# Optimization experiments

Measured on AMD Instinct MI355X. Metric: run time of the kernel, lower is better.

## Reference

```python
import jax, jax.numpy as jnp
import numpy as np

H = 2048
EPS = 1e-5

def _layernorm(x, g, b):
    mu = jnp.mean(x, axis=-1, keepdims=True)
    var = jnp.mean(jnp.square(x - mu), axis=-1, keepdims=True)
    return (x - mu) * jax.lax.rsqrt(var + EPS) * g + b

def setup_inputs() -> dict:
    key = jax.random.key(0)
    ks = jax.random.split(key, 12)
    s = 1.0 / np.sqrt(H)
    inp = {
        "x": jax.random.normal(ks[0], (2, 2048, H), dtype=jnp.float32),
        "ln1_g": jnp.ones((H,), jnp.float32),
        "ln1_b": jnp.zeros((H,), jnp.float32),
        "ln2_g": jnp.ones((H,), jnp.float32),
        "ln2_b": jnp.zeros((H,), jnp.float32),
        "qkv_w": jax.random.uniform(ks[1], (H, 3 * H), jnp.float32, -s, s),
        "qkv_b": jax.random.uniform(ks[2], (3 * H,), jnp.float32, -s, s),
        "out_w": jax.random.uniform(ks[3], (H, H), jnp.float32, -s, s),
        "out_b": jax.random.uniform(ks[4], (H,), jnp.float32, -s, s),
        "mlp_w1": jax.random.uniform(ks[5], (H, 4 * H), jnp.float32, -s, s),
        "mlp_b1": jax.random.uniform(ks[6], (4 * H,), jnp.float32, -s, s),
        "mlp_w2": jax.random.uniform(ks[7], (4 * H, H), jnp.float32, -1.0 / np.sqrt(4 * H), 1.0 / np.sqrt(4 * H)),
        "mlp_b2": jax.random.uniform(ks[8], (H,), jnp.float32, -1.0 / np.sqrt(4 * H), 1.0 / np.sqrt(4 * H)),
    }
    return inp

def reference(x, ln1_g, ln1_b, ln2_g, ln2_b, qkv_w, qkv_b, out_w, out_b, mlp_w1, mlp_b1, mlp_w2, mlp_b2):
    residual = x
    h = _layernorm(x, ln1_g, ln1_b)
    qkv = h @ qkv_w + qkv_b                      # [B,S,3H]
    q, k, v = jnp.split(qkv, 3, axis=-1)         # each [B,S,H] (single-head attention)
    scores = jnp.einsum('bsh,bth->bst', q, k) / jnp.sqrt(jnp.float32(H))
    attn = jax.nn.softmax(scores, axis=-1)
    attn_out = jnp.einsum('bst,bth->bsh', attn, v)
    attn_out = attn_out @ out_w + out_b
    x = residual + attn_out                      # dropout is identity in eval
    residual = x
    h = _layernorm(x, ln2_g, ln2_b)
    h = jax.nn.gelu(h @ mlp_w1 + mlp_b1, approximate=False)
    h = h @ mlp_w2 + mlp_b2
    return residual + h
```

## Files before the change

### kernel.cpp

```cpp
#include <hip/hip_runtime.h>
#include <hip/hip_bf16.h>
#include <math.h>

typedef __bf16 bf16_t;
typedef __bf16 bf16x8 __attribute__((ext_vector_type(8)));
typedef __bf16 bf16x4 __attribute__((ext_vector_type(4)));
typedef float  f32x4  __attribute__((ext_vector_type(4)));

enum { EPI_BF16_BIAS = 0, EPI_F32_SCALE = 1, EPI_BF16 = 2, EPI_F32_BIAS_RES = 3, EPI_BF16_BIAS_GELU = 4 };

__device__ __forceinline__ float gelu_exact(float v) {
  return 0.5f * v * (1.0f + erff(v * 0.7071067811865476f));
}

__device__ __forceinline__ void gld_lds16(const bf16_t* g, bf16_t* l) {
  __builtin_amdgcn_global_load_lds(
      (const __attribute__((address_space(1))) uint32_t*)(uintptr_t)g,
      (__attribute__((address_space(3))) uint32_t*)(uintptr_t)l, 16, 0, 0);
}

#define SB()    __builtin_amdgcn_s_barrier()
#define SCHED() __builtin_amdgcn_sched_barrier(0)
#define VMW0()  asm volatile("s_waitcnt vmcnt(0)" ::: "memory")

#define RD(base, rowbase, ks) \
  (*(const bf16x8*)((base) + ((rowbase) + lr) * 64 + (((((ks) << 2) | lg)) ^ (lr & 7)) * 8))

template<int EPI>
__global__ __launch_bounds__(512, 2) void tb_gemm8(
    const bf16_t* __restrict__ A, int lda, long long strideA,
    const bf16_t* __restrict__ B, int ldb, long long strideB,
    const float* __restrict__ bias,
    const float* __restrict__ resid,
    void* __restrict__ Cp, int ldc, long long strideC,
    int K, float scale)
{
  __shared__ __align__(16) bf16_t sm[65536];

  const int tid = threadIdx.x;
  const int lane = tid & 63;
  const int wid = tid >> 6;
  const int wm = wid >> 2;
  const int wn = wid & 3;
  const int lr = lane & 15;
  const int lg = lane >> 4;
  const int z = blockIdx.z;
  const int m0 = blockIdx.y * 256;
  const int n0 = blockIdx.x * 256;

  const bf16_t* Ag = A + (size_t)z * strideA + (size_t)m0 * lda;
  const bf16_t* Bg = B + (size_t)z * strideB + (size_t)n0 * ldb;

  const int l3 = lane >> 3;
  const int sl8 = ((lane & 7) ^ l3) << 3;

  f32x4 acc[8][4];
#pragma unroll
  for (int i = 0; i < 8; ++i)
#pragma unroll
    for (int j = 0; j < 4; ++j) acc[i][j] = (f32x4){0.f, 0.f, 0.f, 0.f};

  auto stage = [&](int par, int kt) {
    bf16_t* da = sm + (par << 15);
    bf16_t* db = da + 16384;
#pragma unroll
    for (int h = 0; h < 2; ++h)
#pragma unroll
      for (int q = 0; q < 2; ++q) {
        int c = (wid << 1) + q;
        int row = (h << 7) + (c << 3) + l3;
        gld_lds16(Ag + (size_t)row * lda + kt + sl8, da + (h << 13) + (c << 9) + lane * 8);
        gld_lds16(Bg + (size_t)row * ldb + kt + sl8, db + (h << 13) + (c << 9) + lane * 8);
      }
  };

  const int NT = K >> 6;
  stage(0, 0);
  VMW0();
  SB();

  for (int t = 0; t < NT; ++t) {
    SCHED();
    const bf16_t* cura = sm + ((t & 1) << 15);
    const bf16_t* curb = cura + 16384;
    if (t + 1 < NT) stage((t + 1) & 1, (t + 1) << 6);

    bf16x8 bF[4][2], aF[4][2];
#pragma unroll
    for (int jj = 0; jj < 4; ++jj) {
      bF[jj][0] = RD(curb, jj * 64 + wn * 16, 0);
      bF[jj][1] = RD(curb, jj * 64 + wn * 16, 1);
    }
#pragma unroll
    for (int ii = 0; ii < 4; ++ii) {
      aF[ii][0] = RD(cura, ii * 32 + wm * 16, 0);
      aF[ii][1] = RD(cura, ii * 32 + wm * 16, 1);
    }
    __builtin_amdgcn_s_setprio(1);
#pragma unroll
    for (int ii = 0; ii < 4; ++ii)
#pragma unroll
      for (int jj = 0; jj < 4; ++jj)
#pragma unroll
        for (int ks = 0; ks < 2; ++ks)
          acc[ii][jj] = __builtin_amdgcn_mfma_f32_16x16x32_bf16(aF[ii][ks], bF[jj][ks], acc[ii][jj], 0, 0, 0);
    __builtin_amdgcn_s_setprio(0);
#pragma unroll
    for (int ii = 0; ii < 4; ++ii) {
      aF[ii][0] = RD(cura, 128 + ii * 32 + wm * 16, 0);
      aF[ii][1] = RD(cura, 128 + ii * 32 + wm * 16, 1);
    }
    __builtin_amdgcn_s_setprio(1);
#pragma unroll
    for (int ii = 0; ii < 4; ++ii)
#pragma unroll
      for (int jj = 0; jj < 4; ++jj)
#pragma unroll
        for (int ks = 0; ks < 2; ++ks)
          acc[4 + ii][jj] = __builtin_amdgcn_mfma_f32_16x16x32_bf16(aF[ii][ks], bF[jj][ks], acc[4 + ii][jj], 0, 0, 0);
    __builtin_amdgcn_s_setprio(0);

    SCHED();
    if (t + 1 < NT) {
      VMW0();
      SB();
    }
  }

#pragma unroll
  for (int i = 0; i < 8; ++i) {
    const int mr = ((i >> 2) << 7) + ((i & 3) << 5) + (wm << 4);
#pragma unroll
    for (int j = 0; j < 4; ++j) {
      const int nc = j * 64 + (wn << 4);
#pragma unroll
      for (int r = 0; r < 4; ++r) {
        int row = m0 + mr + lg * 4 + r;
        int col = n0 + nc + lr;
        float v = acc[i][j][r] * scale;
        if constexpr (EPI == EPI_BF16_BIAS || EPI == EPI_F32_BIAS_RES || EPI == EPI_BF16_BIAS_GELU)
          v += bias[col];
        if constexpr (EPI == EPI_BF16_BIAS_GELU)
          v = gelu_exact(v);
        if constexpr (EPI == EPI_F32_BIAS_RES)
          v += resid[(size_t)row * ldc + col];
        if constexpr (EPI == EPI_BF16_BIAS || EPI == EPI_BF16 || EPI == EPI_BF16_BIAS_GELU) {
          ((bf16_t*)Cp)[(size_t)z * strideC + (size_t)row * ldc + col] = (bf16_t)v;
        } else {
          ((float*)Cp)[(size_t)z * strideC + (size_t)row * ldc + col] = v;
        }
      }
    }
  }
}

__global__ __launch_bounds__(256) void tb_combine(
    const float* __restrict__ x2, const float* __restrict__ p0,
    const float* __restrict__ p1, const float* __restrict__ bias,
    float* __restrict__ out)
{
  size_t o = ((size_t)blockIdx.x * 256 + threadIdx.x) * 4;
  float4 a = *(const float4*)(x2 + o);
  float4 b = *(const float4*)(p0 + o);
  float4 c = *(const float4*)(p1 + o);
  float4 bb = *(const float4*)(bias + (o & 2047));
  float4 r;
  r.x = a.x + b.x + c.x + bb.x;
  r.y = a.y + b.y + c.y + bb.y;
  r.z = a.z + b.z + c.z + bb.z;
  r.w = a.w + b.w + c.w + bb.w;
  *(float4*)(out + o) = r;
}

__global__ __launch_bounds__(256) void tb_transpose_cast(
    const float* __restrict__ in, bf16_t* __restrict__ outT, int R, int C)
{
  __shared__ float tile[32][33];
  int c0 = blockIdx.x * 32;
  int r0 = blockIdx.y * 32;
  int t = threadIdx.x;
  int r = t >> 3;
  int c4 = (t & 7) * 4;
  float4 d = *(const float4*)(in + (size_t)(r0 + r) * C + c0 + c4);
  tile[r][c4 + 0] = d.x; tile[r][c4 + 1] = d.y; tile[r][c4 + 2] = d.z; tile[r][c4 + 3] = d.w;
  __syncthreads();
  int c = t >> 3;
  int r4 = (t & 7) * 4;
  bf16x4 o;
  o[0] = (bf16_t)tile[r4 + 0][c];
  o[1] = (bf16_t)tile[r4 + 1][c];
  o[2] = (bf16_t)tile[r4 + 2][c];
  o[3] = (bf16_t)tile[r4 + 3][c];
  *(bf16x4*)(outT + (size_t)(c0 + c) * R + r0 + r4) = o;
}

__global__ __launch_bounds__(256) void tb_transpose_bf16(
    const bf16_t* __restrict__ in, int ldin, long long sIn,
    bf16_t* __restrict__ out, int ldout, long long sOut)
{
  __shared__ bf16_t tile[32][40];
  int z = blockIdx.z;
  const bf16_t* src = in + (size_t)z * sIn;
  bf16_t* dst = out + (size_t)z * sOut;
  int c0 = blockIdx.x * 32;
  int r0 = blockIdx.y * 32;
  int t = threadIdx.x;
  int r = t >> 3;
  int c4 = (t & 7) * 4;
  bf16x4 d = *(const bf16x4*)(src + (size_t)(r0 + r) * ldin + c0 + c4);
  *(bf16x4*)&tile[r][c4] = d;
  __syncthreads();
  int c = t >> 3;
  int r4 = (t & 7) * 4;
  bf16x4 o;
  o[0] = tile[r4 + 0][c];
  o[1] = tile[r4 + 1][c];
  o[2] = tile[r4 + 2][c];
  o[3] = tile[r4 + 3][c];
  *(bf16x4*)(dst + (size_t)(c0 + c) * ldout + r0 + r4) = o;
}

__global__ __launch_bounds__(256) void tb_layernorm(
    const float* __restrict__ x, const float* __restrict__ g, const float* __restrict__ b,
    bf16_t* __restrict__ h)
{
  __shared__ float sa[4], sb[4];
  int row = blockIdx.x;
  int t = threadIdx.x;
  const float* xr = x + (size_t)row * 2048;
  float4 v0 = *(const float4*)(xr + t * 8);
  float4 v1 = *(const float4*)(xr + t * 8 + 4);
  float a[8] = {v0.x, v0.y, v0.z, v0.w, v1.x, v1.y, v1.z, v1.w};
  float s = 0.f, q = 0.f;
#pragma unroll
  for (int j = 0; j < 8; ++j) { s += a[j]; q += a[j] * a[j]; }
#pragma unroll
  for (int o = 32; o; o >>= 1) { s += __shfl_down(s, o); q += __shfl_down(q, o); }
  int w = t >> 6, l = t & 63;
  if (l == 0) { sa[w] = s; sb[w] = q; }
  __syncthreads();
  if (t == 0) {
    sa[0] = sa[0] + sa[1] + sa[2] + sa[3];
    sb[0] = sb[0] + sb[1] + sb[2] + sb[3];
  }
  __syncthreads();
  float mu = sa[0] * (1.0f / 2048.0f);
  float var = sb[0] * (1.0f / 2048.0f) - mu * mu;
  float rs = rsqrtf(var + 1e-5f);
  float4 g0 = *(const float4*)(g + t * 8);
  float4 g1 = *(const float4*)(g + t * 8 + 4);
  float4 b0 = *(const float4*)(b + t * 8);
  float4 b1 = *(const float4*)(b + t * 8 + 4);
  float gv[8] = {g0.x, g0.y, g0.z, g0.w, g1.x, g1.y, g1.z, g1.w};
  float bv[8] = {b0.x, b0.y, b0.z, b0.w, b1.x, b1.y, b1.z, b1.w};
  bf16x8 o8;
#pragma unroll
  for (int j = 0; j < 8; ++j) o8[j] = (bf16_t)((a[j] - mu) * rs * gv[j] + bv[j]);
  *(bf16x8*)(h + (size_t)row * 2048 + t * 8) = o8;
}

__global__ __launch_bounds__(256) void tb_softmax(
    const float* __restrict__ S, bf16_t* __restrict__ P)
{
  __shared__ float sa[4];
  int row = blockIdx.x;
  int t = threadIdx.x;
  const float* sr = S + (size_t)row * 2048;
  float4 a0 = *(const float4*)(sr + t * 8);
  float4 a1 = *(const float4*)(sr + t * 8 + 4);
  float v[8] = {a0.x, a0.y, a0.z, a0.w, a1.x, a1.y, a1.z, a1.w};
  float m = v[0];
#pragma unroll
  for (int j = 1; j < 8; ++j) m = fmaxf(m, v[j]);
#pragma unroll
  for (int o = 32; o; o >>= 1) m = fmaxf(m, __shfl_down(m, o));
  int w = t >> 6, l = t & 63;
  if (l == 0) sa[w] = m;
  __syncthreads();
  if (t == 0) sa[0] = fmaxf(fmaxf(sa[0], sa[1]), fmaxf(sa[2], sa[3]));
  __syncthreads();
  m = sa[0];
  __syncthreads();
  float s = 0.f;
#pragma unroll
  for (int j = 0; j < 8; ++j) { v[j] = expf(v[j] - m); s += v[j]; }
#pragma unroll
  for (int o = 32; o; o >>= 1) s += __shfl_down(s, o);
  if (l == 0) sa[w] = s;
  __syncthreads();
  if (t == 0) sa[0] = sa[0] + sa[1] + sa[2] + sa[3];
  __syncthreads();
  float inv = 1.0f / sa[0];
  bf16x8 o8;
#pragma unroll
  for (int j = 0; j < 8; ++j) o8[j] = (bf16_t)(v[j] * inv);
  *(bf16x8*)(P + (size_t)row * 2048 + t * 8) = o8;
}

extern "C" void kernel_launch(void* const* d_in, const int* in_sizes, int n_in,
                              void* d_out, int out_size, void* d_ws, size_t ws_size,
                              hipStream_t stream) {
  const float* x     = (const float*)d_in[0];
  const float* ln1_g = (const float*)d_in[1];
  const float* ln1_b = (const float*)d_in[2];
  const float* ln2_g = (const float*)d_in[3];
  const float* ln2_b = (const float*)d_in[4];
  const float* qkv_w = (const float*)d_in[5];
  const float* qkv_b = (const float*)d_in[6];
  const float* out_w = (const float*)d_in[7];
  const float* out_b = (const float*)d_in[8];
  const float* w1    = (const float*)d_in[9];
  const float* b1    = (const float*)d_in[10];
  const float* w2    = (const float*)d_in[11];
  const float* b2    = (const float*)d_in[12];
  float* out = (float*)d_out;
  char* ws = (char*)d_ws;

  bf16_t* qkv_wT = (bf16_t*)(ws + 0);
  bf16_t* out_wT = (bf16_t*)(ws + 25165824);
  bf16_t* w1T    = (bf16_t*)(ws + 33554432);
  bf16_t* w2T    = (bf16_t*)(ws + 67108864);
  bf16_t* h_bf   = (bf16_t*)(ws + 100663296);
  bf16_t* qkv_bf = (bf16_t*)(ws + 117440512);
  float*  scores = (float*)(ws + 167772160);
  bf16_t* attn_bf= (bf16_t*)(ws + 201326592);
  bf16_t* ao_bf  = (bf16_t*)(ws + 218103808);
  float*  x2     = (float*)(ws + 234881024);
  bf16_t* mid_bf = (bf16_t*)(ws + 117440512);
  bf16_t* Vt     = (bf16_t*)(ws + 234881024);
  float*  part0  = (float*)(ws + 0);
  float*  part1  = (float*)(ws + 201326592);

  const float inv_sqrt_h = 0.022097086912079608f;

  tb_transpose_cast<<<dim3(6144 / 32, 2048 / 32), 256, 0, stream>>>(qkv_w, qkv_wT, 2048, 6144);
  tb_transpose_cast<<<dim3(2048 / 32, 2048 / 32), 256, 0, stream>>>(out_w, out_wT, 2048, 2048);
  tb_transpose_cast<<<dim3(8192 / 32, 2048 / 32), 256, 0, stream>>>(w1, w1T, 2048, 8192);
  tb_transpose_cast<<<dim3(2048 / 32, 8192 / 32), 256, 0, stream>>>(w2, w2T, 8192, 2048);

  tb_layernorm<<<4096, 256, 0, stream>>>(x, ln1_g, ln1_b, h_bf);

  tb_gemm8<EPI_BF16_BIAS><<<dim3(24, 16, 1), 512, 0, stream>>>(
      h_bf, 2048, 0, qkv_wT, 2048, 0, qkv_b, nullptr, qkv_bf, 6144, 0, 2048, 1.0f);

  tb_transpose_bf16<<<dim3(64, 64, 2), 256, 0, stream>>>(
      qkv_bf + 4096, 6144, 2048LL * 6144, Vt, 2048, 2048LL * 2048);

  tb_gemm8<EPI_F32_SCALE><<<dim3(8, 8, 2), 512, 0, stream>>>(
      qkv_bf, 6144, 2048LL * 6144, qkv_bf + 2048, 6144, 2048LL * 6144,
      nullptr, nullptr, scores, 2048, 2048LL * 2048, 2048, inv_sqrt_h);

  tb_softmax<<<4096, 256, 0, stream>>>(scores, attn_bf);

  tb_gemm8<EPI_BF16><<<dim3(8, 8, 2), 512, 0, stream>>>(
      attn_bf, 2048, 2048LL * 2048, Vt, 2048, 2048LL * 2048,
      nullptr, nullptr, ao_bf, 2048, 2048LL * 2048, 2048, 1.0f);

  tb_gemm8<EPI_F32_BIAS_RES><<<dim3(8, 16, 1), 512, 0, stream>>>(
      ao_bf, 2048, 0, out_wT, 2048, 0, out_b, x, x2, 2048, 0, 2048, 1.0f);

  tb_layernorm<<<4096, 256, 0, stream>>>(x2, ln2_g, ln2_b, h_bf);

  tb_gemm8<EPI_BF16_BIAS_GELU><<<dim3(32, 16, 1), 512, 0, stream>>>(
      h_bf, 2048, 0, w1T, 2048, 0, b1, nullptr, mid_bf, 8192, 0, 2048, 1.0f);

  tb_gemm8<EPI_F32_SCALE><<<dim3(8, 16, 2), 512, 0, stream>>>(
      mid_bf, 8192, 4096, w2T, 8192, 4096,
      nullptr, nullptr, part0, 2048, 50331648LL, 4096, 1.0f);

  tb_combine<<<8192, 256, 0, stream>>>(x2, part0, part1, b2, out);
}
```

Measured before the change: 734.5 us.

## Switch GEMM to a 4-stage LDS ring with K-tile 32 and unswizzled layout

Replaces the double-buffered 64-wide K pipeline with a four-slot ring of 32-wide K tiles, keeping three global-to-LDS loads in flight. Partial vmcnt waits (8/4/0) replace the full drain each step. The goal is to hide global-load latency better. In exchange it drops the XOR swizzle, so LDS reads may hit bank conflicts. It also issues twice as many barriers per unit of K.

```diff
diff --git a/kernel.cpp b/kernel.cpp
--- a/kernel.cpp
+++ b/kernel.cpp
@@ -21,10 +21,9 @@
 
 #define SB()    __builtin_amdgcn_s_barrier()
 #define SCHED() __builtin_amdgcn_sched_barrier(0)
+#define VMW8()  asm volatile("s_waitcnt vmcnt(8)" ::: "memory")
+#define VMW4()  asm volatile("s_waitcnt vmcnt(4)" ::: "memory")
 #define VMW0()  asm volatile("s_waitcnt vmcnt(0)" ::: "memory")
-
-#define RD(base, rowbase, ks) \
-  (*(const bf16x8*)((base) + ((rowbase) + lr) * 64 + (((((ks) << 2) | lg)) ^ (lr & 7)) * 8))
 
 template<int EPI>
 __global__ __launch_bounds__(512, 2) void tb_gemm8(
@@ -51,8 +50,8 @@
   const bf16_t* Ag = A + (size_t)z * strideA + (size_t)m0 * lda;
   const bf16_t* Bg = B + (size_t)z * strideB + (size_t)n0 * ldb;
 
-  const int l3 = lane >> 3;
-  const int sl8 = ((lane & 7) ^ l3) << 3;
+  const int srow = lane >> 2;
+  const int scol = (lane & 3) * 8;
 
   f32x4 acc[8][4];
 #pragma unroll
@@ -60,70 +59,52 @@
 #pragma unroll
     for (int j = 0; j < 4; ++j) acc[i][j] = (f32x4){0.f, 0.f, 0.f, 0.f};
 
-  auto stage = [&](int par, int kt) {
-    bf16_t* da = sm + (par << 15);
-    bf16_t* db = da + 16384;
-#pragma unroll
-    for (int h = 0; h < 2; ++h)
-#pragma unroll
-      for (int q = 0; q < 2; ++q) {
-        int c = (wid << 1) + q;
-        int row = (h << 7) + (c << 3) + l3;
-        gld_lds16(Ag + (size_t)row * lda + kt + sl8, da + (h << 13) + (c << 9) + lane * 8);
-        gld_lds16(Bg + (size_t)row * ldb + kt + sl8, db + (h << 13) + (c << 9) + lane * 8);
-      }
+  auto stage = [&](bf16_t* buf, int kt) {
+#pragma unroll
+    for (int q = 0; q < 2; ++q) {
+      int c = (wid << 1) + q;
+      int row = (c << 4) + srow;
+      gld_lds16(Ag + (size_t)row * lda + kt + scol, buf + (c << 9) + lane * 8);
+      gld_lds16(Bg + (size_t)row * ldb + kt + scol, buf + 8192 + (c << 9) + lane * 8);
+    }
   };
 
-  const int NT = K >> 6;
-  stage(0, 0);
-  VMW0();
+  const int NT = K >> 5;
+  stage(sm, 0);
+  stage(sm + 16384, 32);
+  stage(sm + 32768, 64);
+  VMW8();
   SB();
 
-  for (int t = 0; t < NT; ++t) {
-    SCHED();
-    const bf16_t* cura = sm + ((t & 1) << 15);
-    const bf16_t* curb = cura + 16384;
-    if (t + 1 < NT) stage((t + 1) & 1, (t + 1) << 6);
-
-    bf16x8 bF[4][2], aF[4][2];
-#pragma unroll
-    for (int jj = 0; jj < 4; ++jj) {
-      bF[jj][0] = RD(curb, jj * 64 + wn * 16, 0);
-      bF[jj][1] = RD(curb, jj * 64 + wn * 16, 1);
-    }
-#pragma unroll
-    for (int ii = 0; ii < 4; ++ii) {
-      aF[ii][0] = RD(cura, ii * 32 + wm * 16, 0);
-      aF[ii][1] = RD(cura, ii * 32 + wm * 16, 1);
-    }
-    __builtin_amdgcn_s_setprio(1);
-#pragma unroll
-    for (int ii = 0; ii < 4; ++ii)
+  for (int tb = 0; tb < NT; tb += 4) {
+#pragma unroll
+    for (int u = 0; u < 4; ++u) {
+      const int t = tb + u;
+      const bf16_t* ab = sm + u * 16384;
+      const bf16_t* bb = ab + 8192;
+      if (t + 3 < NT) stage(sm + ((u + 3) & 3) * 16384, (t + 3) << 5);
+
+      bf16x8 aF[8], bF[4];
 #pragma unroll
       for (int jj = 0; jj < 4; ++jj)
-#pragma unroll
-        for (int ks = 0; ks < 2; ++ks)
-          acc[ii][jj] = __builtin_amdgcn_mfma_f32_16x16x32_bf16(aF[ii][ks], bF[jj][ks], acc[ii][jj], 0, 0, 0);
-    __builtin_amdgcn_s_setprio(0);
-#pragma unroll
-    for (int ii = 0; ii < 4; ++ii) {
-      aF[ii][0] = RD(cura, 128 + ii * 32 + wm * 16, 0);
-      aF[ii][1] = RD(cura, 128 + ii * 32 + wm * 16, 1);
-    }
-    __builtin_amdgcn_s_setprio(1);
-#pragma unroll
-    for (int ii = 0; ii < 4; ++ii)
-#pragma unroll
-      for (int jj = 0; jj < 4; ++jj)
-#pragma unroll
-        for (int ks = 0; ks < 2; ++ks)
-          acc[4 + ii][jj] = __builtin_amdgcn_mfma_f32_16x16x32_bf16(aF[ii][ks], bF[jj][ks], acc[4 + ii][jj], 0, 0, 0);
-    __builtin_amdgcn_s_setprio(0);
-
-    SCHED();
-    if (t + 1 < NT) {
-      VMW0();
-      SB();
+        bF[jj] = *(const bf16x8*)&bb[(jj * 64 + wn * 16 + lr) * 32 + lg * 8];
+#pragma unroll
+      for (int ii = 0; ii < 8; ++ii)
+        aF[ii] = *(const bf16x8*)&ab[((((ii >> 2) << 7) + ((ii & 3) << 5) + (wm << 4)) + lr) * 32 + lg * 8];
+
+      __builtin_amdgcn_s_setprio(1);
+#pragma unroll
+      for (int ii = 0; ii < 8; ++ii)
+#pragma unroll
+        for (int jj = 0; jj < 4; ++jj)
+          acc[ii][jj] = __builtin_amdgcn_mfma_f32_16x16x32_bf16(aF[ii], bF[jj], acc[ii][jj], 0, 0, 0);
+      __builtin_amdgcn_s_setprio(0);
+
+      SCHED();
+      if (t + 3 < NT)      { VMW8(); SB(); }
+      else if (t == NT - 3) { VMW4(); SB(); }
+      else if (t == NT - 2) { VMW0(); SB(); }
+      SCHED();
     }
   }
 
```

After: 868.9 us. 1.18x slower.

## Split-K the attention and output-projection GEMMs to fill more CUs

Applied to the files above, without the earlier changes.

Adds a ZDIV template parameter to the GEMM so the z grid dimension covers batch times K-split, with per-split K offsets. QK^T, PV and the output projection now run as 2-way split-K with fp32 partial outputs. The partials are summed in softmax (now tb_softmax_add), in a new tb_combine_pv kernel, and in tb_combine for the residual. The aim is more workgroups on the small 64/128-tile grids for better CU occupancy, at the cost of extra fp32 partial traffic, an extra combine launch, and a rearranged workspace.

```diff
diff --git a/kernel.cpp b/kernel.cpp
--- a/kernel.cpp
+++ b/kernel.cpp
@@ -23,13 +23,10 @@
 #define SCHED() __builtin_amdgcn_sched_barrier(0)
 #define VMW0()  asm volatile("s_waitcnt vmcnt(0)" ::: "memory")
 
-#define RD(base, rowbase, ks) \
-  (*(const bf16x8*)((base) + ((rowbase) + lr) * 64 + (((((ks) << 2) | lg)) ^ (lr & 7)) * 8))
-
-template<int EPI>
+template<int EPI, int ZDIV>
 __global__ __launch_bounds__(512, 2) void tb_gemm8(
-    const bf16_t* __restrict__ A, int lda, long long strideA,
-    const bf16_t* __restrict__ B, int ldb, long long strideB,
+    const bf16_t* __restrict__ A, int lda, long long strideA, long long kofA,
+    const bf16_t* __restrict__ B, int ldb, long long strideB, long long kofB,
     const float* __restrict__ bias,
     const float* __restrict__ resid,
     void* __restrict__ Cp, int ldc, long long strideC,
@@ -45,11 +42,13 @@
   const int lr = lane & 15;
   const int lg = lane >> 4;
   const int z = blockIdx.z;
+  const int batch = z / ZDIV;
+  const int ks = z % ZDIV;
   const int m0 = blockIdx.y * 256;
   const int n0 = blockIdx.x * 256;
 
-  const bf16_t* Ag = A + (size_t)z * strideA + (size_t)m0 * lda;
-  const bf16_t* Bg = B + (size_t)z * strideB + (size_t)n0 * ldb;
+  const bf16_t* Ag = A + (size_t)batch * strideA + (size_t)ks * kofA + (size_t)m0 * lda;
+  const bf16_t* Bg = B + (size_t)batch * strideB + (size_t)ks * kofB + (size_t)n0 * ldb;
 
   const int l3 = lane >> 3;
   const int sl8 = ((lane & 7) ^ l3) << 3;
@@ -74,6 +73,9 @@
       }
   };
 
+#define RD(base, rowbase, kslot) \
+  (*(const bf16x8*)((base) + ((rowbase) + lr) * 64 + (((((kslot) << 2) | lg)) ^ (lr & 7)) * 8))
+
   const int NT = K >> 6;
   stage(0, 0);
   VMW0();
@@ -102,8 +104,8 @@
 #pragma unroll
       for (int jj = 0; jj < 4; ++jj)
 #pragma unroll
-        for (int ks = 0; ks < 2; ++ks)
-          acc[ii][jj] = __builtin_amdgcn_mfma_f32_16x16x32_bf16(aF[ii][ks], bF[jj][ks], acc[ii][jj], 0, 0, 0);
+        for (int kk = 0; kk < 2; ++kk)
+          acc[ii][jj] = __builtin_amdgcn_mfma_f32_16x16x32_bf16(aF[ii][kk], bF[jj][kk], acc[ii][jj], 0, 0, 0);
     __builtin_amdgcn_s_setprio(0);
 #pragma unroll
     for (int ii = 0; ii < 4; ++ii) {
@@ -116,8 +118,8 @@
 #pragma unroll
       for (int jj = 0; jj < 4; ++jj)
 #pragma unroll
-        for (int ks = 0; ks < 2; ++ks)
-          acc[4 + ii][jj] = __builtin_amdgcn_mfma_f32_16x16x32_bf16(aF[ii][ks], bF[jj][ks], acc[4 + ii][jj], 0, 0, 0);
+        for (int kk = 0; kk < 2; ++kk)
+          acc[4 + ii][jj] = __builtin_amdgcn_mfma_f32_16x16x32_bf16(aF[ii][kk], bF[jj][kk], acc[4 + ii][jj], 0, 0, 0);
     __builtin_amdgcn_s_setprio(0);
 
     SCHED();
@@ -126,6 +128,7 @@
       SB();
     }
   }
+#undef RD
 
 #pragma unroll
   for (int i = 0; i < 8; ++i) {
@@ -172,6 +175,24 @@
   *(float4*)(out + o) = r;
 }
 
+__global__ __launch_bounds__(256) void tb_combine_pv(
+    const float* __restrict__ p, bf16_t* __restrict__ ao)
+{
+  size_t o = ((size_t)blockIdx.x * 256 + threadIdx.x) * 4;
+  size_t b = o >> 22;
+  size_t w = o & 4194303;
+  const float* p0 = p + (b << 1) * 4194304 + w;
+  const float* p1 = p0 + 4194304;
+  float4 a = *(const float4*)p0;
+  float4 c = *(const float4*)p1;
+  bf16x4 r;
+  r[0] = (bf16_t)(a.x + c.x);
+  r[1] = (bf16_t)(a.y + c.y);
+  r[2] = (bf16_t)(a.z + c.z);
+  r[3] = (bf16_t)(a.w + c.w);
+  *(bf16x4*)(ao + o) = r;
+}
+
 __global__ __launch_bounds__(256) void tb_transpose_cast(
     const float* __restrict__ in, bf16_t* __restrict__ outT, int R, int C)
 {
@@ -259,16 +280,21 @@
   *(bf16x8*)(h + (size_t)row * 2048 + t * 8) = o8;
 }
 
-__global__ __launch_bounds__(256) void tb_softmax(
-    const float* __restrict__ S, bf16_t* __restrict__ P)
+__global__ __launch_bounds__(256) void tb_softmax_add(
+    const float* __restrict__ p, bf16_t* __restrict__ P)
 {
   __shared__ float sa[4];
   int row = blockIdx.x;
   int t = threadIdx.x;
-  const float* sr = S + (size_t)row * 2048;
-  float4 a0 = *(const float4*)(sr + t * 8);
-  float4 a1 = *(const float4*)(sr + t * 8 + 4);
-  float v[8] = {a0.x, a0.y, a0.z, a0.w, a1.x, a1.y, a1.z, a1.w};
+  size_t base = ((size_t)(row >> 11) * 2) * 4194304 + (size_t)(row & 2047) * 2048;
+  const float* p0 = p + base;
+  const float* p1 = p0 + 4194304;
+  float4 a0 = *(const float4*)(p0 + t * 8);
+  float4 a1 = *(const float4*)(p0 + t * 8 + 4);
+  float4 c0 = *(const float4*)(p1 + t * 8);
+  float4 c1 = *(const float4*)(p1 + t * 8 + 4);
+  float v[8] = {a0.x + c0.x, a0.y + c0.y, a0.z + c0.z, a0.w + c0.w,
+                a1.x + c1.x, a1.y + c1.y, a1.z + c1.z, a1.w + c1.w};
   float m = v[0];
 #pragma unroll
   for (int j = 1; j < 8; ++j) m = fmaxf(m, v[j]);
@@ -316,20 +342,18 @@
   float* out = (float*)d_out;
   char* ws = (char*)d_ws;
 
+  float*  sp     = (float*)(ws + 0);
   bf16_t* qkv_wT = (bf16_t*)(ws + 0);
-  bf16_t* out_wT = (bf16_t*)(ws + 25165824);
-  bf16_t* w1T    = (bf16_t*)(ws + 33554432);
-  bf16_t* w2T    = (bf16_t*)(ws + 67108864);
-  bf16_t* h_bf   = (bf16_t*)(ws + 100663296);
-  bf16_t* qkv_bf = (bf16_t*)(ws + 117440512);
-  float*  scores = (float*)(ws + 167772160);
-  bf16_t* attn_bf= (bf16_t*)(ws + 201326592);
-  bf16_t* ao_bf  = (bf16_t*)(ws + 218103808);
-  float*  x2     = (float*)(ws + 234881024);
-  bf16_t* mid_bf = (bf16_t*)(ws + 117440512);
-  bf16_t* Vt     = (bf16_t*)(ws + 234881024);
-  float*  part0  = (float*)(ws + 0);
-  float*  part1  = (float*)(ws + 201326592);
+  bf16_t* out_wT = (bf16_t*)(ws + 67108864);
+  bf16_t* w1T    = (bf16_t*)(ws + 75497472);
+  bf16_t* w2T    = (bf16_t*)(ws + 109051904);
+  bf16_t* h_bf   = (bf16_t*)(ws + 142606336);
+  bf16_t* qkv_bf = (bf16_t*)(ws + 159383552);
+  bf16_t* mid_bf = (bf16_t*)(ws + 159383552);
+  bf16_t* attn_bf= (bf16_t*)(ws + 209715200);
+  bf16_t* Vt     = (bf16_t*)(ws + 226492416);
+  bf16_t* ao_bf  = (bf16_t*)(ws + 243269632);
+  float*  x2     = (float*)(ws + 226492416);
 
   const float inv_sqrt_h = 0.022097086912079608f;
 
@@ -340,33 +364,38 @@
 
   tb_layernorm<<<4096, 256, 0, stream>>>(x, ln1_g, ln1_b, h_bf);
 
-  tb_gemm8<EPI_BF16_BIAS><<<dim3(24, 16, 1), 512, 0, stream>>>(
-      h_bf, 2048, 0, qkv_wT, 2048, 0, qkv_b, nullptr, qkv_bf, 6144, 0, 2048, 1.0f);
+  tb_gemm8<EPI_BF16_BIAS, 1><<<dim3(24, 16, 1), 512, 0, stream>>>(
+      h_bf, 2048, 0, 0, qkv_wT, 2048, 0, 0, qkv_b, nullptr, qkv_bf, 6144, 0, 2048, 1.0f);
 
   tb_transpose_bf16<<<dim3(64, 64, 2), 256, 0, stream>>>(
       qkv_bf + 4096, 6144, 2048LL * 6144, Vt, 2048, 2048LL * 2048);
 
-  tb_gemm8<EPI_F32_SCALE><<<dim3(8, 8, 2), 512, 0, stream>>>(
-      qkv_bf, 6144, 2048LL * 6144, qkv_bf + 2048, 6144, 2048LL * 6144,
-      nullptr, nullptr, scores, 2048, 2048LL * 2048, 2048, inv_sqrt_h);
-
-  tb_softmax<<<4096, 256, 0, stream>>>(scores, attn_bf);
-
-  tb_gemm8<EPI_BF16><<<dim3(8, 8, 2), 512, 0, stream>>>(
-      attn_bf, 2048, 2048LL * 2048, Vt, 2048, 2048LL * 2048,
-      nullptr, nullptr, ao_bf, 2048, 2048LL * 2048, 2048, 1.0f);
-
-  tb_gemm8<EPI_F32_BIAS_RES><<<dim3(8, 16, 1), 512, 0, stream>>>(
-      ao_bf, 2048, 0, out_wT, 2048, 0, out_b, x, x2, 2048, 0, 2048, 1.0f);
+  tb_gemm8<EPI_F32_SCALE, 2><<<dim3(8, 8, 4), 512, 0, stream>>>(
+      qkv_bf, 6144, 2048LL * 6144, 1024, qkv_bf + 2048, 6144, 2048LL * 6144, 1024,
+      nullptr, nullptr, sp, 2048, 4194304LL, 1024, inv_sqrt_h);
+
+  tb_softmax_add<<<4096, 256, 0, stream>>>(sp, attn_bf);
+
+  tb_gemm8<EPI_F32_SCALE, 2><<<dim3(8, 8, 4), 512, 0, stream>>>(
+      attn_bf, 2048, 2048LL * 2048, 1024, Vt, 2048, 2048LL * 2048, 1024,
+      nullptr, nullptr, sp, 2048, 4194304LL, 1024, 1.0f);
+
+  tb_combine_pv<<<8192, 256, 0, stream>>>(sp, ao_bf);
+
+  tb_gemm8<EPI_F32_SCALE, 2><<<dim3(8, 16, 2), 512, 0, stream>>>(
+      ao_bf, 2048, 0, 1024, out_wT, 2048, 0, 1024,
+      nullptr, nullptr, sp, 2048, 8388608LL, 1024, 1.0f);
+
+  tb_combine<<<8192, 256, 0, stream>>>(x, sp, sp + 8388608, out_b, x2);
 
   tb_layernorm<<<4096, 256, 0, stream>>>(x2, ln2_g, ln2_b, h_bf);
 
-  tb_gemm8<EPI_BF16_BIAS_GELU><<<dim3(32, 16, 1), 512, 0, stream>>>(
-      h_bf, 2048, 0, w1T, 2048, 0, b1, nullptr, mid_bf, 8192, 0, 2048, 1.0f);
-
-  tb_gemm8<EPI_F32_SCALE><<<dim3(8, 16, 2), 512, 0, stream>>>(
-      mid_bf, 8192, 4096, w2T, 8192, 4096,
-      nullptr, nullptr, part0, 2048, 50331648LL, 4096, 1.0f);
-
-  tb_combine<<<8192, 256, 0, stream>>>(x2, part0, part1, b2, out);
-}
+  tb_gemm8<EPI_BF16_BIAS_GELU, 1><<<dim3(32, 16, 1), 512, 0, stream>>>(
+      h_bf, 2048, 0, 0, w1T, 2048, 0, 0, b1, nullptr, mid_bf, 8192, 0, 2048, 1.0f);
+
+  tb_gemm8<EPI_F32_SCALE, 2><<<dim3(8, 16, 2), 512, 0, stream>>>(
+      mid_bf, 8192, 0, 4096, w2T, 8192, 0, 4096,
+      nullptr, nullptr, sp, 2048, 8388608LL, 4096, 1.0f);
+
+  tb_combine<<<8192, 256, 0, stream>>>(x2, sp, sp + 8388608, b2, out);
+}
```

Result: faster. 686.3 us (-6.6%).
